# Optimization experiments

Hardware: AMD Instinct MI355X
Metric: run time of the kernel (lower is better)

The kernel has to match this reference:

```python
import jax, jax.numpy as jnp
import numpy as np

L, E, H, T, B = 8, 1024, 16, 2048, 1
DH = E // H
LN_EPS = 1e-5
MASKED_BIAS = -10000.0


def setup_inputs() -> dict:
    key = jax.random.key(0)
    ks = jax.random.split(key, 6)
    std = 0.02
    return {
        "x": jax.random.normal(ks[0], (B, T, E), jnp.float32),
        "ln1_w": jnp.ones((L, E), jnp.float32),
        "ln1_b": jnp.zeros((L, E), jnp.float32),
        "attn_w": std * jax.random.normal(ks[1], (L, E, 3 * E), jnp.float32),
        "attn_b": jnp.zeros((L, 3 * E), jnp.float32),
        "proj_w": std * jax.random.normal(ks[2], (L, E, E), jnp.float32),
        "proj_b": jnp.zeros((L, E), jnp.float32),
        "ln2_w": jnp.ones((L, E), jnp.float32),
        "ln2_b": jnp.zeros((L, E), jnp.float32),
        "fc_w": std * jax.random.normal(ks[3], (L, E, 4 * E), jnp.float32),
        "fc_b": jnp.zeros((L, 4 * E), jnp.float32),
        "fc2_w": std * jax.random.normal(ks[4], (L, 4 * E, E), jnp.float32),
        "fc2_b": jnp.zeros((L, E), jnp.float32),
    }


def _layernorm(h, w, b):
    mu = jnp.mean(h, axis=-1, keepdims=True)
    var = jnp.mean(jnp.square(h - mu), axis=-1, keepdims=True)
    return (h - mu) * jax.lax.rsqrt(var + LN_EPS) * w + b


def _gpt2_stack(x, ln1_w, ln1_b, attn_w, attn_b, proj_w, proj_b,
                ln2_w, ln2_b, fc_w, fc_b, fc2_w, fc2_b):
    b, t, e = x.shape
    causal = jnp.tril(jnp.ones((t, t), dtype=bool))  # [T,T] tril mask buffer
    scale = 1.0 / jnp.sqrt(jnp.float32(DH))          # scale=True -> 1/sqrt(head_dim)

    def block(h, p):
        l1w, l1b, aw, ab, pw, pb, l2w, l2b, fw, fb, f2w, f2b = p
        # masked self-attention
        y = _layernorm(h, l1w, l1b)
        qkv = y @ aw + ab                              # [B,T,3E]
        q, k, v = jnp.split(qkv, 3, axis=-1)
        sh = lambda z: z.reshape(b, t, H, DH).transpose(0, 2, 1, 3)  # [B,H,T,DH]
        q, k, v = sh(q), sh(k), sh(v)
        w = jnp.einsum("bhqd,bhkd->bhqk", q, k) * scale
        w = jnp.where(causal, w, jnp.float32(MASKED_BIAS))
        w = jax.nn.softmax(w, axis=-1)
        a = jnp.einsum("bhqk,bhkd->bhqd", w, v)
        a = a.transpose(0, 2, 1, 3).reshape(b, t, e)   # merge heads
        a = a @ pw + pb
        h = h + a
        # MLP (gelu_new = tanh-approx gelu)
        y = _layernorm(h, l2w, l2b)
        m = jax.nn.gelu(y @ fw + fb, approximate=True) @ f2w + f2b
        return h + m, None

    out, _ = jax.lax.scan(
        block, x,
        (ln1_w, ln1_b, attn_w, attn_b, proj_w, proj_b,
         ln2_w, ln2_b, fc_w, fc_b, fc2_w, fc2_b))
    return out


def reference(x, ln1_w, ln1_b, attn_w, attn_b, proj_w, proj_b,
              ln2_w, ln2_b, fc_w, fc_b, fc2_w, fc2_b):
    return _gpt2_stack(x, ln1_w, ln1_b, attn_w, attn_b, proj_w, proj_b,
                       ln2_w, ln2_b, fc_w, fc_b, fc2_w, fc2_b)
```

## Files before the change

kernel.cpp:

```cpp
#include <hip/hip_runtime.h>
#include <cstdint>

typedef short s16x8 __attribute__((ext_vector_type(8)));
typedef __bf16 b16x8 __attribute__((ext_vector_type(8)));
typedef float f32x4 __attribute__((ext_vector_type(4)));

#define TSEQ 2048
#define EDIM 1024

__device__ __forceinline__ short f2bf(float x) {
  unsigned u = __float_as_uint(x);
  unsigned r = (u + 0x7FFFu + ((u >> 16) & 1u)) >> 16;
  return (short)r;
}

__device__ __forceinline__ f32x4 mfma16(s16x8 a, s16x8 b, f32x4 c) {
  return __builtin_amdgcn_mfma_f32_16x16x32_bf16(
      __builtin_bit_cast(b16x8, a), __builtin_bit_cast(b16x8, b), c, 0, 0, 0);
}

__device__ __forceinline__ void gl_lds16(void* lds, const void* g) {
  __builtin_amdgcn_global_load_lds(
      (const __attribute__((address_space(1))) void*)g,
      (__attribute__((address_space(3))) void*)lds, 16, 0, 0);
}

__global__ __launch_bounds__(256) void cvtT(
    const float* __restrict__ W, short* __restrict__ WT, int K, int N) {
  int t = blockIdx.x;
  const int tn = N >> 5;
  const int bn = (t % tn) << 5, bk = (t / tn) << 5;
  __shared__ float tile[32][33];
  const int tx = threadIdx.x & 31, ty = threadIdx.x >> 5;
#pragma unroll
  for (int i = 0; i < 4; ++i)
    tile[ty + i * 8][tx] = W[(size_t)(bk + ty + i * 8) * N + bn + tx];
  __syncthreads();
#pragma unroll
  for (int i = 0; i < 4; ++i)
    WT[(size_t)(bn + ty + i * 8) * K + bk + tx] = f2bf(tile[tx][ty + i * 8]);
}

__global__ __launch_bounds__(256) void ln_kernel(
    const float* __restrict__ h, const float* __restrict__ w,
    const float* __restrict__ b, short* __restrict__ y) {
  const int row = blockIdx.x, tid = threadIdx.x;
  const float4 v = ((const float4*)(h + (size_t)row * EDIM))[tid];
  float s = v.x + v.y + v.z + v.w;
  float s2 = v.x * v.x + v.y * v.y + v.z * v.z + v.w * v.w;
#pragma unroll
  for (int off = 1; off < 64; off <<= 1) {
    s += __shfl_xor(s, off, 64);
    s2 += __shfl_xor(s2, off, 64);
  }
  __shared__ float red[8];
  const int wave = tid >> 6, lane = tid & 63;
  if (lane == 0) { red[wave] = s; red[4 + wave] = s2; }
  __syncthreads();
  s = red[0] + red[1] + red[2] + red[3];
  s2 = red[4] + red[5] + red[6] + red[7];
  const float mu = s * (1.f / EDIM);
  const float var = s2 * (1.f / EDIM) - mu * mu;
  const float rstd = rsqrtf(var + 1e-5f);
  const float4 wv = ((const float4*)w)[tid];
  const float4 bv = ((const float4*)b)[tid];
  short4 o = make_short4(f2bf((v.x - mu) * rstd * wv.x + bv.x),
                         f2bf((v.y - mu) * rstd * wv.y + bv.y),
                         f2bf((v.z - mu) * rstd * wv.z + bv.z),
                         f2bf((v.w - mu) * rstd * wv.w + bv.w));
  ((short4*)(y + (size_t)row * EDIM))[tid] = o;
}

template <int EPI, int BM>
__global__ __launch_bounds__(256, 2) void gemm_bt(
    const short* __restrict__ A, const short* __restrict__ BT,
    const float* __restrict__ bias, short* __restrict__ out_bf,
    short* __restrict__ vt, float* __restrict__ out_f,
    int M, int N, int K) {
  constexpr int WM = BM / 2;
  constexpr int NMI = WM / 16;
  constexpr int ASZ = BM * 64;
  constexpr int BSZ = 128 * 64;
  __shared__ __align__(16) short As[2 * ASZ];
  __shared__ __align__(16) short Bs[2 * BSZ];
  const int tid = threadIdx.x;
  const int wave = tid >> 6, lane = tid & 63;
  const int quad = lane >> 4, l16 = lane & 15;
  const int wr = (wave >> 1) * WM, wc = (wave & 1) * 64;
  const int m0 = blockIdx.y * BM, n0 = blockIdx.x * 128;
  const int ksplit = K / gridDim.z;
  const int kbase = blockIdx.z * ksplit;

  const int r8 = lane >> 3, c8 = lane & 7;
  const int csw = (c8 ^ r8) << 3;
  const short* Ag = A + (size_t)(m0 + wave * (BM / 4) + r8) * K + kbase + csw;
  const short* Bg = BT + (size_t)(n0 + wave * 32 + r8) * K + kbase + csw;

  f32x4 acc[NMI][4] = {};
  const int NT = ksplit >> 6;

#pragma unroll
  for (int c = 0; c < BM / 32; ++c)
    gl_lds16(&As[(wave * (BM / 32) + c) * 512], Ag + (size_t)(8 * c) * K);
#pragma unroll
  for (int c = 0; c < 4; ++c)
    gl_lds16(&Bs[(wave * 4 + c) * 512], Bg + (size_t)(8 * c) * K);
  __syncthreads();

  int cur = 0;
  for (int t = 0; t < NT; ++t) {
    if (t + 1 < NT) {
      const size_t ko = (size_t)(t + 1) << 6;
#pragma unroll
      for (int c = 0; c < BM / 32; ++c)
        gl_lds16(&As[(cur ^ 1) * ASZ + (wave * (BM / 32) + c) * 512],
                 Ag + (size_t)(8 * c) * K + ko);
#pragma unroll
      for (int c = 0; c < 4; ++c)
        gl_lds16(&Bs[(cur ^ 1) * BSZ + (wave * 4 + c) * 512],
                 Bg + (size_t)(8 * c) * K + ko);
    }
    const short* Ab = &As[cur * ASZ];
    const short* Bb = &Bs[cur * BSZ];
    const int rsw = l16 & 7;
    s16x8 af[NMI][2], bfr[4][2];
#pragma unroll
    for (int i = 0; i < NMI; ++i)
#pragma unroll
      for (int ks = 0; ks < 2; ++ks)
        af[i][ks] = *(const s16x8*)&Ab[(wr + i * 16 + l16) * 64 +
                                       ((((ks << 2) | quad) ^ rsw) << 3)];
#pragma unroll
    for (int i = 0; i < 4; ++i)
#pragma unroll
      for (int ks = 0; ks < 2; ++ks)
        bfr[i][ks] = *(const s16x8*)&Bb[(wc + i * 16 + l16) * 64 +
                                        ((((ks << 2) | quad) ^ rsw) << 3)];
#pragma unroll
    for (int mi = 0; mi < NMI; ++mi)
#pragma unroll
      for (int ni = 0; ni < 4; ++ni)
#pragma unroll
        for (int ks = 0; ks < 2; ++ks)
          acc[mi][ni] = mfma16(af[mi][ks], bfr[ni][ks], acc[mi][ni]);
    __syncthreads();
    cur ^= 1;
  }

#pragma unroll
  for (int mi = 0; mi < NMI; ++mi) {
#pragma unroll
    for (int ni = 0; ni < 4; ++ni) {
      const int col = n0 + wc + ni * 16 + l16;
      const float bv = (EPI == 1 && blockIdx.z != 0) ? 0.f : bias[col];
#pragma unroll
      for (int r = 0; r < 4; ++r) {
        const int row = m0 + wr + mi * 16 + quad * 4 + r;
        float v = acc[mi][ni][r] + bv;
        if (EPI == 1) {
          atomicAdd(&out_f[(size_t)row * N + col], v);
        } else if (EPI == 2) {
          const float u = 0.7978845608028654f * (v + 0.044715f * v * v * v);
          const float e = __expf(2.f * u);
          const float th = 1.f - 2.f / (e + 1.f);
          out_bf[(size_t)row * N + col] = f2bf(0.5f * v * (1.f + th));
        } else {
          if (col < 2048)
            out_bf[(size_t)row * 2048 + col] = f2bf(v);
          else
            vt[(size_t)(col - 2048) * TSEQ + row] = f2bf(v);
        }
      }
    }
  }
}

__global__ __launch_bounds__(256) void attn_fused(
    const short* __restrict__ qk,
    const short* __restrict__ vt,
    short* __restrict__ aout) {
  const int head = blockIdx.y;
  const int sidx = (blockIdx.x + 4 * (head & 7)) & 31;
  const int qg = (head < 8) ? sidx : 31 - sidx;
  const int qbase = qg << 6;
  const int qt_end = qg >> 1;

  const int tid = threadIdx.x;
  const int wave = tid >> 6, lane = tid & 63;
  const int quad = lane >> 4, l16 = lane & 15;
  const int qrow = qbase + wave * 16;

  __shared__ __align__(16) short Ks[128 * 64];
  __shared__ __align__(16) short Vs[64 * 128];
  __shared__ __align__(16) short ps[4][16 * 136];
  short* psw = ps[wave];

  s16x8 qf[2];
#pragma unroll
  for (int ks = 0; ks < 2; ++ks)
    qf[ks] = *(const s16x8*)&qk[(size_t)(qrow + l16) * 2048 +
                                head * 64 + ks * 32 + quad * 8];

  const int krow_off = tid >> 3;
  const int kchk = ((tid & 7) ^ (krow_off & 7)) * 8;
  const int vrow_off = tid >> 4;
  const int vchk = ((tid & 15) ^ vrow_off) * 8;

  const float scale = 0.125f;
  float mrow[4], lrow[4];
  f32x4 oacc[4] = {};
#pragma unroll
  for (int r = 0; r < 4; ++r) { mrow[r] = -1e30f; lrow[r] = 0.f; }

  for (int kt = 0; kt <= qt_end; ++kt) {
    const int k0 = kt << 7;
#pragma unroll
    for (int c = 0; c < 4; ++c) {
      gl_lds16(&Ks[c * 2048 + wave * 512],
               qk + (size_t)(k0 + c * 32 + krow_off) * 2048 + 1024 + head * 64 + kchk);
      gl_lds16(&Vs[c * 2048 + wave * 512],
               vt + (size_t)(head * 64 + c * 16 + vrow_off) * TSEQ + k0 + vchk);
    }
    __syncthreads();

    f32x4 s[8] = {};
    __builtin_amdgcn_s_setprio(1);
#pragma unroll
    for (int ni = 0; ni < 8; ++ni) {
      const int kr = ni * 16 + l16;
      const int sw = kr & 7;
      s16x8 kf0 = *(const s16x8*)((const char*)Ks + kr * 128 + ((quad ^ sw) << 4));
      s16x8 kf1 = *(const s16x8*)((const char*)Ks + kr * 128 + ((quad ^ 4 ^ sw) << 4));
      s[ni] = mfma16(qf[0], kf0, s[ni]);
      s[ni] = mfma16(qf[1], kf1, s[ni]);
    }
    __builtin_amdgcn_s_setprio(0);

    const bool diag = (kt == qt_end);
    float rmax[4] = {-1e30f, -1e30f, -1e30f, -1e30f};
#pragma unroll
    for (int ni = 0; ni < 8; ++ni)
#pragma unroll
      for (int r = 0; r < 4; ++r) {
        float v = s[ni][r] * scale;
        if (diag) {
          const int qa = qrow + quad * 4 + r;
          const int ka = k0 + ni * 16 + l16;
          if (ka > qa) v = -1e30f;
        }
        s[ni][r] = v;
        rmax[r] = fmaxf(rmax[r], v);
      }
#pragma unroll
    for (int off = 1; off < 16; off <<= 1)
#pragma unroll
      for (int r = 0; r < 4; ++r)
        rmax[r] = fmaxf(rmax[r], __shfl_xor(rmax[r], off, 64));
    float al[4];
#pragma unroll
    for (int r = 0; r < 4; ++r) {
      const float mnew = fmaxf(mrow[r], rmax[r]);
      al[r] = __expf(mrow[r] - mnew);
      mrow[r] = mnew;
      lrow[r] *= al[r];
    }
#pragma unroll
    for (int ni = 0; ni < 4; ++ni)
#pragma unroll
      for (int r = 0; r < 4; ++r) oacc[ni][r] *= al[r];
    float psum[4] = {};
#pragma unroll
    for (int ni = 0; ni < 8; ++ni)
#pragma unroll
      for (int r = 0; r < 4; ++r) {
        const float p = __expf(s[ni][r] - mrow[r]);
        psum[r] += p;
        psw[(quad * 4 + r) * 136 + ni * 16 + l16] = f2bf(p);
      }
#pragma unroll
    for (int off = 1; off < 16; off <<= 1)
#pragma unroll
      for (int r = 0; r < 4; ++r) psum[r] += __shfl_xor(psum[r], off, 64);
#pragma unroll
    for (int r = 0; r < 4; ++r) lrow[r] += psum[r];

    __builtin_amdgcn_s_setprio(1);
#pragma unroll
    for (int ks = 0; ks < 4; ++ks) {
      s16x8 pa = *(const s16x8*)&psw[l16 * 136 + ks * 32 + quad * 8];
#pragma unroll
      for (int ni = 0; ni < 4; ++ni) {
        const int vr = ni * 16 + l16;
        s16x8 vf = *(const s16x8*)((const char*)Vs + vr * 256 +
                                   ((((ks << 2) | quad) ^ (vr & 15)) << 4));
        oacc[ni] = mfma16(pa, vf, oacc[ni]);
      }
    }
    __builtin_amdgcn_s_setprio(0);
    __syncthreads();
  }

#pragma unroll
  for (int ni = 0; ni < 4; ++ni)
#pragma unroll
    for (int r = 0; r < 4; ++r) {
      const int qa = qrow + quad * 4 + r;
      aout[(size_t)qa * EDIM + head * 64 + ni * 16 + l16] =
          f2bf(oacc[ni][r] / lrow[r]);
    }
}

extern "C" void kernel_launch(void* const* d_in, const int* in_sizes, int n_in,
                              void* d_out, int out_size, void* d_ws, size_t ws_size,
                              hipStream_t stream) {
  const float* x     = (const float*)d_in[0];
  const float* ln1w  = (const float*)d_in[1];
  const float* ln1b  = (const float*)d_in[2];
  const float* attw  = (const float*)d_in[3];
  const float* attb  = (const float*)d_in[4];
  const float* projw = (const float*)d_in[5];
  const float* projb = (const float*)d_in[6];
  const float* ln2w  = (const float*)d_in[7];
  const float* ln2b  = (const float*)d_in[8];
  const float* fcw   = (const float*)d_in[9];
  const float* fcb   = (const float*)d_in[10];
  const float* fc2w  = (const float*)d_in[11];
  const float* fc2b  = (const float*)d_in[12];

  char* ws = (char*)d_ws;
  float* h   = (float*)(ws);
  short* y   = (short*)(ws + (8u << 20));
  short* att = (short*)(ws + (8u << 20));
  short* qkb = (short*)(ws + (12u << 20));
  short* vt  = (short*)(ws + (20u << 20));
  short* mid = (short*)(ws + (12u << 20));
  short* wT  = (short*)(ws + (28u << 20));

  hipMemcpyAsync(h, x, (size_t)TSEQ * EDIM * 4, hipMemcpyDeviceToDevice, stream);

  for (int l = 0; l < 8; ++l) {
    ln_kernel<<<TSEQ, 256, 0, stream>>>(h, ln1w + l * 1024, ln1b + l * 1024, y);
    cvtT<<<(3072 / 32) * (1024 / 32), 256, 0, stream>>>(
        attw + (size_t)l * 1024 * 3072, wT, 1024, 3072);
    gemm_bt<0, 128><<<dim3(24, 16, 1), 256, 0, stream>>>(
        y, wT, attb + l * 3072, qkb, vt, nullptr, 2048, 3072, 1024);
    attn_fused<<<dim3(32, 16), 256, 0, stream>>>(qkb, vt, att);
    cvtT<<<(1024 / 32) * (1024 / 32), 256, 0, stream>>>(
        projw + (size_t)l * 1024 * 1024, wT, 1024, 1024);
    gemm_bt<1, 64><<<dim3(8, 32, 2), 256, 0, stream>>>(
        att, wT, projb + l * 1024, nullptr, nullptr, h, 2048, 1024, 1024);
    ln_kernel<<<TSEQ, 256, 0, stream>>>(h, ln2w + l * 1024, ln2b + l * 1024, y);
    cvtT<<<(4096 / 32) * (1024 / 32), 256, 0, stream>>>(
        fcw + (size_t)l * 1024 * 4096, wT, 1024, 4096);
    gemm_bt<2, 128><<<dim3(32, 16, 1), 256, 0, stream>>>(
        y, wT, fcb + l * 4096, mid, nullptr, nullptr, 2048, 4096, 1024);
    cvtT<<<(1024 / 32) * (4096 / 32), 256, 0, stream>>>(
        fc2w + (size_t)l * 4096 * 1024, wT, 4096, 1024);
    gemm_bt<1, 64><<<dim3(8, 32, 2), 256, 0, stream>>>(
        mid, wT, fc2b + l * 1024, nullptr, nullptr, h, 2048, 1024, 4096);
  }

  hipMemcpyAsync(d_out, h, (size_t)TSEQ * EDIM * 4, hipMemcpyDeviceToDevice, stream);
}
```

Baseline: 1.827 ms.

## Use 32x32x16 MFMA in GEMM and batch weight conversion up front

The GEMM inner loop now issues 32x32x16 bf16 MFMAs instead of 16x16x32, which changes fragment loads and the epilogue row mapping. This cuts LDS fragment reads per flop and the instruction count. Separately, all eight layers' weights are transposed and converted to bf16 in four batched launches before the layer loop, replacing 32 per-layer conversion launches. The weights are still converted every call, so there is no cross-call caching, but the workspace now needs room for every layer's converted weights at once.

Result: slower. 1.875 ms (+2.6%).

```diff
diff --git a/kernel.cpp b/kernel.cpp
--- a/kernel.cpp
+++ b/kernel.cpp
@@ -4,6 +4,7 @@
 typedef short s16x8 __attribute__((ext_vector_type(8)));
 typedef __bf16 b16x8 __attribute__((ext_vector_type(8)));
 typedef float f32x4 __attribute__((ext_vector_type(4)));
+typedef float f32x16 __attribute__((ext_vector_type(16)));
 
 #define TSEQ 2048
 #define EDIM 1024
@@ -19,14 +20,21 @@
       __builtin_bit_cast(b16x8, a), __builtin_bit_cast(b16x8, b), c, 0, 0, 0);
 }
 
+__device__ __forceinline__ f32x16 mfma32(s16x8 a, s16x8 b, f32x16 c) {
+  return __builtin_amdgcn_mfma_f32_32x32x16_bf16(
+      __builtin_bit_cast(b16x8, a), __builtin_bit_cast(b16x8, b), c, 0, 0, 0);
+}
+
 __device__ __forceinline__ void gl_lds16(void* lds, const void* g) {
   __builtin_amdgcn_global_load_lds(
       (const __attribute__((address_space(1))) void*)g,
       (__attribute__((address_space(3))) void*)lds, 16, 0, 0);
 }
 
-__global__ __launch_bounds__(256) void cvtT(
-    const float* __restrict__ W, short* __restrict__ WT, int K, int N) {
+__global__ __launch_bounds__(256) void cvtTL(
+    const float* __restrict__ W0, short* __restrict__ WT0, int K, int N) {
+  const float* W = W0 + (size_t)blockIdx.y * K * N;
+  short* WT = WT0 + (size_t)blockIdx.y * K * N;
   int t = blockIdx.x;
   const int tn = N >> 5;
   const int bn = (t % tn) << 5, bk = (t / tn) << 5;
@@ -78,14 +86,14 @@
     short* __restrict__ vt, float* __restrict__ out_f,
     int M, int N, int K) {
   constexpr int WM = BM / 2;
-  constexpr int NMI = WM / 16;
+  constexpr int NMI = WM / 32;
   constexpr int ASZ = BM * 64;
   constexpr int BSZ = 128 * 64;
   __shared__ __align__(16) short As[2 * ASZ];
   __shared__ __align__(16) short Bs[2 * BSZ];
   const int tid = threadIdx.x;
   const int wave = tid >> 6, lane = tid & 63;
-  const int quad = lane >> 4, l16 = lane & 15;
+  const int l32 = lane & 31, kh = lane >> 5, rsw = l32 & 7;
   const int wr = (wave >> 1) * WM, wc = (wave & 1) * 64;
   const int m0 = blockIdx.y * BM, n0 = blockIdx.x * 128;
   const int ksplit = K / gridDim.z;
@@ -96,7 +104,7 @@
   const short* Ag = A + (size_t)(m0 + wave * (BM / 4) + r8) * K + kbase + csw;
   const short* Bg = BT + (size_t)(n0 + wave * 32 + r8) * K + kbase + csw;
 
-  f32x4 acc[NMI][4] = {};
+  f32x16 acc[NMI][2] = {};
   const int NT = ksplit >> 6;
 
 #pragma unroll
@@ -122,27 +130,22 @@
     }
     const short* Ab = &As[cur * ASZ];
     const short* Bb = &Bs[cur * BSZ];
-    const int rsw = l16 & 7;
-    s16x8 af[NMI][2], bfr[4][2];
-#pragma unroll
-    for (int i = 0; i < NMI; ++i)
-#pragma unroll
-      for (int ks = 0; ks < 2; ++ks)
-        af[i][ks] = *(const s16x8*)&Ab[(wr + i * 16 + l16) * 64 +
-                                       ((((ks << 2) | quad) ^ rsw) << 3)];
-#pragma unroll
-    for (int i = 0; i < 4; ++i)
-#pragma unroll
-      for (int ks = 0; ks < 2; ++ks)
-        bfr[i][ks] = *(const s16x8*)&Bb[(wc + i * 16 + l16) * 64 +
-                                        ((((ks << 2) | quad) ^ rsw) << 3)];
-#pragma unroll
-    for (int mi = 0; mi < NMI; ++mi)
-#pragma unroll
-      for (int ni = 0; ni < 4; ++ni)
-#pragma unroll
-        for (int ks = 0; ks < 2; ++ks)
-          acc[mi][ni] = mfma16(af[mi][ks], bfr[ni][ks], acc[mi][ni]);
+#pragma unroll
+    for (int ks = 0; ks < 4; ++ks) {
+      const int chk = ((ks * 2 + kh) ^ rsw) << 3;
+      s16x8 af[NMI], bfv[2];
+#pragma unroll
+      for (int mi = 0; mi < NMI; ++mi)
+        af[mi] = *(const s16x8*)&Ab[(wr + mi * 32 + l32) * 64 + chk];
+#pragma unroll
+      for (int ni = 0; ni < 2; ++ni)
+        bfv[ni] = *(const s16x8*)&Bb[(wc + ni * 32 + l32) * 64 + chk];
+#pragma unroll
+      for (int mi = 0; mi < NMI; ++mi)
+#pragma unroll
+        for (int ni = 0; ni < 2; ++ni)
+          acc[mi][ni] = mfma32(af[mi], bfv[ni], acc[mi][ni]);
+    }
     __syncthreads();
     cur ^= 1;
   }
@@ -150,12 +153,12 @@
 #pragma unroll
   for (int mi = 0; mi < NMI; ++mi) {
 #pragma unroll
-    for (int ni = 0; ni < 4; ++ni) {
-      const int col = n0 + wc + ni * 16 + l16;
+    for (int ni = 0; ni < 2; ++ni) {
+      const int col = n0 + wc + ni * 32 + l32;
       const float bv = (EPI == 1 && blockIdx.z != 0) ? 0.f : bias[col];
 #pragma unroll
-      for (int r = 0; r < 4; ++r) {
-        const int row = m0 + wr + mi * 16 + quad * 4 + r;
+      for (int r = 0; r < 16; ++r) {
+        const int row = m0 + wr + mi * 32 + (r & 3) + 8 * (r >> 2) + 4 * kh;
         float v = acc[mi][ni][r] + bv;
         if (EPI == 1) {
           atomicAdd(&out_f[(size_t)row * N + col], v);
@@ -334,30 +337,34 @@
   short* qkb = (short*)(ws + (12u << 20));
   short* vt  = (short*)(ws + (20u << 20));
   short* mid = (short*)(ws + (12u << 20));
-  short* wT  = (short*)(ws + (28u << 20));
+  short* attnT = (short*)(ws + (36u << 20));
+  short* projT = attnT + (size_t)8 * 3072 * 1024;
+  short* fcT   = projT + (size_t)8 * 1024 * 1024;
+  short* fc2T  = fcT + (size_t)8 * 1024 * 4096;
 
   hipMemcpyAsync(h, x, (size_t)TSEQ * EDIM * 4, hipMemcpyDeviceToDevice, stream);
+
+  cvtTL<<<dim3((3072 / 32) * (1024 / 32), 8), 256, 0, stream>>>(attw, attnT, 1024, 3072);
+  cvtTL<<<dim3((1024 / 32) * (1024 / 32), 8), 256, 0, stream>>>(projw, projT, 1024, 1024);
+  cvtTL<<<dim3((4096 / 32) * (1024 / 32), 8), 256, 0, stream>>>(fcw, fcT, 1024, 4096);
+  cvtTL<<<dim3((1024 / 32) * (4096 / 32), 8), 256, 0, stream>>>(fc2w, fc2T, 4096, 1024);
 
   for (int l = 0; l < 8; ++l) {
     ln_kernel<<<TSEQ, 256, 0, stream>>>(h, ln1w + l * 1024, ln1b + l * 1024, y);
-    cvtT<<<(3072 / 32) * (1024 / 32), 256, 0, stream>>>(
-        attw + (size_t)l * 1024 * 3072, wT, 1024, 3072);
     gemm_bt<0, 128><<<dim3(24, 16, 1), 256, 0, stream>>>(
-        y, wT, attb + l * 3072, qkb, vt, nullptr, 2048, 3072, 1024);
+        y, attnT + (size_t)l * 3072 * 1024, attb + l * 3072, qkb, vt, nullptr,
+        2048, 3072, 1024);
     attn_fused<<<dim3(32, 16), 256, 0, stream>>>(qkb, vt, att);
-    cvtT<<<(1024 / 32) * (1024 / 32), 256, 0, stream>>>(
-        projw + (size_t)l * 1024 * 1024, wT, 1024, 1024);
     gemm_bt<1, 64><<<dim3(8, 32, 2), 256, 0, stream>>>(
-        att, wT, projb + l * 1024, nullptr, nullptr, h, 2048, 1024, 1024);
+        att, projT + (size_t)l * 1024 * 1024, projb + l * 1024, nullptr, nullptr,
+        h, 2048, 1024, 1024);
     ln_kernel<<<TSEQ, 256, 0, stream>>>(h, ln2w + l * 1024, ln2b + l * 1024, y);
-    cvtT<<<(4096 / 32) * (1024 / 32), 256, 0, stream>>>(
-        fcw + (size_t)l * 1024 * 4096, wT, 1024, 4096);
     gemm_bt<2, 128><<<dim3(32, 16, 1), 256, 0, stream>>>(
-        y, wT, fcb + l * 4096, mid, nullptr, nullptr, 2048, 4096, 1024);
-    cvtT<<<(1024 / 32) * (4096 / 32), 256, 0, stream>>>(
-        fc2w + (size_t)l * 4096 * 1024, wT, 4096, 1024);
+        y, fcT + (size_t)l * 4096 * 1024, fcb + l * 4096, mid, nullptr, nullptr,
+        2048, 4096, 1024);
     gemm_bt<1, 64><<<dim3(8, 32, 2), 256, 0, stream>>>(
-        mid, wT, fc2b + l * 1024, nullptr, nullptr, h, 2048, 1024, 4096);
+        mid, fc2T + (size_t)l * 4096 * 1024, fc2b + l * 1024, nullptr, nullptr,
+        h, 2048, 1024, 4096);
   }
 
   hipMemcpyAsync(d_out, h, (size_t)TSEQ * EDIM * 4, hipMemcpyDeviceToDevice, stream);
```
